# Kernel tuning notes

Measured on AMD Instinct MI355X. Metric: run time of the kernel, lower is better.

The kernel has to match this reference:

```python
import jax, jax.numpy as jnp
import numpy as np

D_MODEL = 1024
NUM_HEADS = 16
DEPTH = D_MODEL // NUM_HEADS  # 64
B, S = 4, 2048
NEG_BIG = -1000000000.0


def setup_inputs() -> dict:
    key = jax.random.key(0)
    ks = jax.random.split(key, 9)
    # Glorot-uniform per-head projection weights, stacked over heads: [H, d_model, depth]
    lim_qkv = np.sqrt(6.0 / (D_MODEL + DEPTH)).astype(np.float32)
    lim_o = np.sqrt(6.0 / (D_MODEL + D_MODEL)).astype(np.float32)
    x = jax.random.normal(ks[0], (B, S, D_MODEL), dtype=jnp.float32)
    attention_mask = jnp.ones((B, S, 1), dtype=jnp.float32)
    Wq = jax.random.uniform(ks[1], (NUM_HEADS, D_MODEL, DEPTH), jnp.float32, -lim_qkv, lim_qkv)
    Wk = jax.random.uniform(ks[2], (NUM_HEADS, D_MODEL, DEPTH), jnp.float32, -lim_qkv, lim_qkv)
    Wv = jax.random.uniform(ks[3], (NUM_HEADS, D_MODEL, DEPTH), jnp.float32, -lim_qkv, lim_qkv)
    bq = jnp.zeros((NUM_HEADS, DEPTH), jnp.float32)
    bk = jnp.zeros((NUM_HEADS, DEPTH), jnp.float32)
    bv = jnp.zeros((NUM_HEADS, DEPTH), jnp.float32)
    Wo = jax.random.uniform(ks[4], (D_MODEL, D_MODEL), jnp.float32, -lim_o, lim_o)
    bo = jnp.zeros((D_MODEL,), jnp.float32)
    return {"x": x, "attention_mask": attention_mask, "Wq": Wq, "bq": bq,
            "Wk": Wk, "bk": bk, "Wv": Wv, "bv": bv, "Wo": Wo, "bo": bo}


def reference(x, attention_mask, Wq, bq, Wk, bk, Wv, bv, Wo, bo):
    # Batched over heads (same math as the per-head Python loop + concat).
    # x: [B,S,D]; Wq/Wk/Wv: [H,D,depth]; bq/bk/bv: [H,depth]
    q = jnp.einsum('bsd,hde->bhse', x, Wq) + bq[None, :, None, :]
    k = jnp.einsum('bsd,hde->bhse', x, Wk) + bk[None, :, None, :]
    v = jnp.einsum('bsd,hde->bhse', x, Wv) + bv[None, :, None, :]
    scale = 1.0 / jnp.sqrt(jnp.asarray(DEPTH, dtype=x.dtype))
    scores = jnp.einsum('bhse,bhte->bhst', q, k) * scale  # [B,H,S,S]
    # original: mask.transpose(-2,-1) -> [B,1,S], broadcast over query rows; add head axis
    mask_t = jnp.swapaxes(attention_mask, -2, -1)[:, None]  # [B,1,1,S]
    scores = scores + (1.0 - mask_t) * NEG_BIG
    probs = jax.nn.softmax(scores, axis=-1)
    z = jnp.einsum('bhst,bhte->bhse', probs, v)  # [B,H,S,depth]
    # concat heads along feature dim (head order matches torch.cat order)
    multi_head = jnp.transpose(z, (0, 2, 1, 3)).reshape(x.shape[0], x.shape[1], NUM_HEADS * DEPTH)
    return multi_head @ Wo + bo
```

## Files before the change

### kernel.cpp

```cpp
#include <hip/hip_runtime.h>

#define NH 16
#define DEP 64
#define DM 1024
#define BB 4
#define SS 2048

typedef __attribute__((ext_vector_type(8))) __bf16 bf16x8;
typedef __attribute__((ext_vector_type(4))) __bf16 bf16x4;
typedef __attribute__((ext_vector_type(2))) __bf16 bf16x2;
typedef __attribute__((ext_vector_type(4))) float f32x4;
typedef __attribute__((ext_vector_type(4))) unsigned u32x4;
typedef __attribute__((ext_vector_type(2))) unsigned u32x2;
typedef unsigned short u16;

#define MFMA_BF16(A, B, C) __builtin_amdgcn_mfma_f32_16x16x32_bf16(A, B, C, 0, 0, 0)

#define SCL 0.18033688011112042f
#define LOG2E 1.4426950408889634f

__device__ __forceinline__ u16 f2bf(float f) {
  unsigned u = __builtin_bit_cast(unsigned, f);
  u += 0x7fffu + ((u >> 16) & 1u);
  return (u16)(u >> 16);
}

__device__ __forceinline__ unsigned pk2(float a, float b) {
  bf16x2 t;
  t[0] = (__bf16)a; t[1] = (__bf16)b;
  return __builtin_bit_cast(unsigned, t);
}

__device__ __forceinline__ void gload_lds16(const u16* g, u16* l) {
  __builtin_amdgcn_global_load_lds((const __attribute__((address_space(1))) void*)g,
                                   (__attribute__((address_space(3))) void*)l, 16, 0, 0);
}

__global__ __launch_bounds__(256) void k_cvt_x(const float* __restrict__ x, u16* __restrict__ xb) {
  int i = (blockIdx.x * 256 + threadIdx.x) * 4;
  float4 v = *(const float4*)(x + i);
  ushort4 o;
  o.x = f2bf(v.x); o.y = f2bf(v.y); o.z = f2bf(v.z); o.w = f2bf(v.w);
  *(ushort4*)(xb + i) = o;
}

__global__ __launch_bounds__(256) void k_pack_qkv(const float* __restrict__ Wq, const float* __restrict__ Wk,
                                                  const float* __restrict__ Wv,
                                                  const float* __restrict__ bq, const float* __restrict__ bk,
                                                  const float* __restrict__ bv,
                                                  u16* __restrict__ wt, float* __restrict__ biasN) {
  __shared__ float lt[64][65];
  int k0 = blockIdx.x * 64;
  int z = blockIdx.y;
  int which = z >> 4, h = z & 15;
  const float* W = which == 0 ? Wq : (which == 1 ? Wk : Wv);
  const float* bsrc = which == 0 ? bq : (which == 1 ? bk : bv);
  const float* src = W + (size_t)h * DM * DEP;
  int t = threadIdx.x;
#pragma unroll
  for (int p = 0; p < 16; ++p) {
    int li = p * 256 + t;
    int r = li >> 6, c = li & 63;
    lt[r][c] = src[(size_t)(k0 + r) * 64 + c];
  }
  __syncthreads();
  int woff = which * DM + h * 64;
#pragma unroll
  for (int p = 0; p < 16; ++p) {
    int li = p * 256 + t;
    int r = li >> 6, c = li & 63;
    wt[(size_t)(woff + r) * DM + k0 + c] = f2bf(lt[c][r]);
  }
  if (blockIdx.x == 0 && t < 64) biasN[woff + t] = bsrc[h * 64 + t];
}

__global__ __launch_bounds__(256) void k_pack_wo(const float* __restrict__ Wo, u16* __restrict__ wot) {
  __shared__ float lt[64][65];
  int k0 = blockIdx.x * 64, n0 = blockIdx.y * 64;
  int t = threadIdx.x;
#pragma unroll
  for (int p = 0; p < 16; ++p) {
    int li = p * 256 + t;
    int r = li >> 6, c = li & 63;
    lt[r][c] = Wo[(size_t)(k0 + r) * DM + n0 + c];
  }
  __syncthreads();
#pragma unroll
  for (int p = 0; p < 16; ++p) {
    int li = p * 256 + t;
    int r = li >> 6, c = li & 63;
    wot[(size_t)(n0 + r) * DM + k0 + c] = f2bf(lt[c][r]);
  }
}

__global__ __launch_bounds__(256) void k_maskbias(const float* __restrict__ mask, float* __restrict__ mb) {
  int i = blockIdx.x * 256 + threadIdx.x;
  mb[i] = (1.0f - mask[i]) * (-1000000000.0f * LOG2E);
}

__global__ __launch_bounds__(256) void k_gemm_qkv(const u16* __restrict__ xb, const u16* __restrict__ wt,
                                                  const float* __restrict__ biasN,
                                                  u16* __restrict__ qb, u16* __restrict__ kb,
                                                  u16* __restrict__ vtb) {
  __shared__ u16 lA[2][128 * 32];
  __shared__ u16 lB[2][128 * 32];
  const int tid = threadIdx.x;
  const int lane = tid & 63, w = tid >> 6;
  const int m0 = blockIdx.x * 128, n0 = blockIdx.y * 128;
  const int wm = (w >> 1) * 64, wn = (w & 1) * 64;
  const int fr = lane & 15, fg = lane >> 4;
  const int bidx = tid * 16;
  const int row0 = bidx >> 6, c0 = (bidx & 63) >> 1;
  f32x4 acc[4][4] = {};
  auto stage = [&](int k0, int buf) {
    gload_lds16(xb + (size_t)(m0 + row0) * DM + k0 + c0, &lA[buf][w * 512]);
    gload_lds16(xb + (size_t)(m0 + row0 + 64) * DM + k0 + c0, &lA[buf][2048 + w * 512]);
    gload_lds16(wt + (size_t)(n0 + row0) * DM + k0 + c0, &lB[buf][w * 512]);
    gload_lds16(wt + (size_t)(n0 + row0 + 64) * DM + k0 + c0, &lB[buf][2048 + w * 512]);
  };
  stage(0, 0);
  __syncthreads();
  for (int k0 = 0; k0 < DM; k0 += 32) {
    const int cur = (k0 >> 5) & 1;
    if (k0 + 32 < DM) stage(k0 + 32, cur ^ 1);
    bf16x8 af[4], bfr[4];
#pragma unroll
    for (int i = 0; i < 4; ++i) {
      af[i] = *(const bf16x8*)&lA[cur][(wm + i * 16 + fr) * 32 + fg * 8];
      bfr[i] = *(const bf16x8*)&lB[cur][(wn + i * 16 + fr) * 32 + fg * 8];
    }
#pragma unroll
    for (int i = 0; i < 4; ++i)
#pragma unroll
      for (int j = 0; j < 4; ++j)
        acc[i][j] = MFMA_BF16(af[i], bfr[j], acc[i][j]);
    __syncthreads();
  }
#pragma unroll
  for (int i = 0; i < 4; ++i)
#pragma unroll
    for (int j = 0; j < 4; ++j) {
      int n = n0 + wn + j * 16 + fr;
      float bn = biasN[n];
      int which = n >> 10, rem = n & 1023, h = rem >> 6, d = rem & 63;
#pragma unroll
      for (int r = 0; r < 4; ++r) {
        int m = m0 + wm + i * 16 + fg * 4 + r;
        int b = m >> 11, s = m & 2047;
        float val = acc[i][j][r] + bn;
        if (which == 0)      qb[(((size_t)(b * NH + h) * SS + s) << 6) + d] = f2bf(val * SCL);
        else if (which == 1) kb[(((size_t)(b * NH + h) * SS + s) << 6) + d] = f2bf(val);
        else                 vtb[(((size_t)(b * NH + h) * 64 + d) << 11) + s] = f2bf(val);
      }
    }
}

__global__ __launch_bounds__(256, 2) void k_attn(const u16* __restrict__ qb, const u16* __restrict__ kb,
                                                 const u16* __restrict__ vtb, const float* __restrict__ mbias,
                                                 u16* __restrict__ zb) {
  __shared__ u16 sK[2][64 * 64];
  __shared__ u16 sV[2][64 * 64];
  const int bid = blockIdx.x;
  const int sw = (bid & 7) * 64 + (bid >> 3);
  const int bh = sw >> 3;
  const int qx = sw & 7;
  const int b = bh >> 4, h = bh & 15;
  const int tid = threadIdx.x, lane = tid & 63, w = tid >> 6;
  const int q0 = qx * 256 + w * 64;
  const u16* Q  = qb  + (size_t)bh * SS * 64;
  const u16* K  = kb  + (size_t)bh * SS * 64;
  const u16* VT = vtb + (size_t)bh * 64 * SS;
  const float* mbb = mbias + b * SS;
  const int fr = lane & 15, fg = lane >> 4;
  const int fr7 = fr & 7;
  const int rsub = lane >> 3;
  const int cg = (lane & 7) ^ rsub;
  const int kc0 = (fg ^ fr7) * 16;
  const int kc1 = ((4 + fg) ^ fr7) * 16;
  const int fg1 = fg >> 1, fgb = (fg & 1) * 8;
  const int cX0 = (((fg1)     ^ fr7)) * 16 + fgb;
  const int cX1 = (((2 + (fg1 ^ 1)) ^ fr7)) * 16 + fgb;
  const int cY0 = (((4 + fg1) ^ fr7)) * 16 + fgb;
  const int cY1 = (((6 + (fg1 ^ 1)) ^ fr7)) * 16 + fgb;
  bf16x8 qlo[4], qhi[4];
#pragma unroll
  for (int qf = 0; qf < 4; ++qf) {
    qlo[qf] = *(const bf16x8*)&Q[(q0 + 16 * qf + fr) * 64 + fg * 8];
    qhi[qf] = *(const bf16x8*)&Q[(q0 + 16 * qf + fr) * 64 + 32 + fg * 8];
  }
  float lrun[4] = {0.f, 0.f, 0.f, 0.f};
  f32x4 o[4][4] = {};

#pragma unroll
  for (int j = 0; j < 2; ++j) {
    int i = w * 2 + j;
    gload_lds16(K + (size_t)(8 * i + rsub) * 64 + cg * 8, &sK[0][i * 512]);
    gload_lds16(VT + (size_t)(8 * i + rsub) * SS + cg * 8, &sV[0][i * 512]);
  }
  __syncthreads();

  for (int t = 0; t < 32; ++t) {
    const int cur = t & 1;
    if (t < 31) {
      const int kvn = (t + 1) * 64;
#pragma unroll
      for (int j = 0; j < 2; ++j) {
        int i = w * 2 + j;
        gload_lds16(K + (size_t)(kvn + 8 * i + rsub) * 64 + cg * 8, &sK[cur ^ 1][i * 512]);
        gload_lds16(VT + (size_t)(8 * i + rsub) * SS + kvn + cg * 8, &sV[cur ^ 1][i * 512]);
      }
    }
    const int kv = t * 64;
    const char* Kb = (const char*)&sK[cur][0];
    const char* Vb = (const char*)&sV[cur][0];
    bf16x8 klo[4], khi[4];
#pragma unroll
    for (int kt = 0; kt < 4; ++kt) {
      klo[kt] = *(const bf16x8*)(Kb + (kt * 16 + fr) * 128 + kc0);
      khi[kt] = *(const bf16x8*)(Kb + (kt * 16 + fr) * 128 + kc1);
    }
    u32x2 vx0[4], vx1[4], vy0[4], vy1[4];
#pragma unroll
    for (int dc = 0; dc < 4; ++dc) {
      const char* rb = Vb + (dc * 16 + fr) * 128;
      vx0[dc] = *(const u32x2*)(rb + cX0);
      vx1[dc] = *(const u32x2*)(rb + cX1);
      vy0[dc] = *(const u32x2*)(rb + cY0);
      vy1[dc] = *(const u32x2*)(rb + cY1);
    }
#pragma unroll
    for (int qf = 0; qf < 4; ++qf) {
      f32x4 sc[4];
      __builtin_amdgcn_s_setprio(1);
#pragma unroll
      for (int kt = 0; kt < 4; ++kt) {
        f32x4 mb4 = *(const f32x4*)(mbb + kv + kt * 16 + fg * 4);
        sc[kt] = MFMA_BF16(khi[kt], qhi[qf], MFMA_BF16(klo[kt], qlo[qf], mb4));
      }
      __builtin_amdgcn_s_setprio(0);
      float e00 = __builtin_amdgcn_exp2f(sc[0][0]), e01 = __builtin_amdgcn_exp2f(sc[0][1]);
      float e02 = __builtin_amdgcn_exp2f(sc[0][2]), e03 = __builtin_amdgcn_exp2f(sc[0][3]);
      float e10 = __builtin_amdgcn_exp2f(sc[1][0]), e11 = __builtin_amdgcn_exp2f(sc[1][1]);
      float e12 = __builtin_amdgcn_exp2f(sc[1][2]), e13 = __builtin_amdgcn_exp2f(sc[1][3]);
      float e20 = __builtin_amdgcn_exp2f(sc[2][0]), e21 = __builtin_amdgcn_exp2f(sc[2][1]);
      float e22 = __builtin_amdgcn_exp2f(sc[2][2]), e23 = __builtin_amdgcn_exp2f(sc[2][3]);
      float e30 = __builtin_amdgcn_exp2f(sc[3][0]), e31 = __builtin_amdgcn_exp2f(sc[3][1]);
      float e32 = __builtin_amdgcn_exp2f(sc[3][2]), e33 = __builtin_amdgcn_exp2f(sc[3][3]);
      lrun[qf] += ((e00 + e01) + (e02 + e03)) + ((e10 + e11) + (e12 + e13))
                + ((e20 + e21) + (e22 + e23)) + ((e30 + e31) + (e32 + e33));
      unsigned w00 = pk2(e00, e01), w01 = pk2(e02, e03);
      unsigned w10 = pk2(e10, e11), w11 = pk2(e12, e13);
      unsigned w20 = pk2(e20, e21), w21 = pk2(e22, e23);
      unsigned w30 = pk2(e30, e31), w31 = pk2(e32, e33);
      unsigned x2 = (unsigned)__shfl_xor((int)w10, 32);
      unsigned x3 = (unsigned)__shfl_xor((int)w11, 32);
      unsigned y2 = (unsigned)__shfl_xor((int)w30, 32);
      unsigned y3 = (unsigned)__shfl_xor((int)w31, 32);
      u32x4 ux = {w00, w01, x2, x3};
      u32x4 uy = {w20, w21, y2, y3};
      bf16x8 paX = __builtin_bit_cast(bf16x8, ux);
      bf16x8 paY = __builtin_bit_cast(bf16x8, uy);
      __builtin_amdgcn_s_setprio(1);
#pragma unroll
      for (int dc = 0; dc < 4; ++dc) {
        u32x4 vxw = {vx0[dc][0], vx0[dc][1], vx1[dc][0], vx1[dc][1]};
        u32x4 vyw = {vy0[dc][0], vy0[dc][1], vy1[dc][0], vy1[dc][1]};
        bf16x8 vX = __builtin_bit_cast(bf16x8, vxw);
        bf16x8 vY = __builtin_bit_cast(bf16x8, vyw);
        o[qf][dc] = MFMA_BF16(paX, vX, o[qf][dc]);
        o[qf][dc] = MFMA_BF16(paY, vY, o[qf][dc]);
      }
      __builtin_amdgcn_s_setprio(0);
    }
    __syncthreads();
  }
#pragma unroll
  for (int qf = 0; qf < 4; ++qf) {
    float l = lrun[qf];
    l += __shfl_xor(l, 16);
    l += __shfl_xor(l, 32);
#pragma unroll
    for (int r = 0; r < 4; ++r) {
      float linv = 1.0f / __shfl(l, 4 * fg + r);
      int s = q0 + 16 * qf + 4 * fg + r;
#pragma unroll
      for (int dc = 0; dc < 4; ++dc)
        zb[(size_t)(b * SS + s) * DM + h * 64 + dc * 16 + fr] = f2bf(o[qf][dc][r] * linv);
    }
  }
}

__global__ __launch_bounds__(256) void k_gemm_out(const u16* __restrict__ zb, const u16* __restrict__ wot,
                                                  const float* __restrict__ bo, float* __restrict__ out) {
  __shared__ u16 lA[2][128 * 32];
  __shared__ u16 lB[2][128 * 32];
  const int tid = threadIdx.x;
  const int lane = tid & 63, w = tid >> 6;
  const int m0 = blockIdx.x * 128, n0 = blockIdx.y * 128;
  const int wm = (w >> 1) * 64, wn = (w & 1) * 64;
  const int fr = lane & 15, fg = lane >> 4;
  const int bidx = tid * 16;
  const int row0 = bidx >> 6, c0 = (bidx & 63) >> 1;
  f32x4 acc[4][4] = {};
  auto stage = [&](int k0, int buf) {
    gload_lds16(zb + (size_t)(m0 + row0) * DM + k0 + c0, &lA[buf][w * 512]);
    gload_lds16(zb + (size_t)(m0 + row0 + 64) * DM + k0 + c0, &lA[buf][2048 + w * 512]);
    gload_lds16(wot + (size_t)(n0 + row0) * DM + k0 + c0, &lB[buf][w * 512]);
    gload_lds16(wot + (size_t)(n0 + row0 + 64) * DM + k0 + c0, &lB[buf][2048 + w * 512]);
  };
  stage(0, 0);
  __syncthreads();
  for (int k0 = 0; k0 < DM; k0 += 32) {
    const int cur = (k0 >> 5) & 1;
    if (k0 + 32 < DM) stage(k0 + 32, cur ^ 1);
    bf16x8 af[4], bfr[4];
#pragma unroll
    for (int i = 0; i < 4; ++i) {
      af[i] = *(const bf16x8*)&lA[cur][(wm + i * 16 + fr) * 32 + fg * 8];
      bfr[i] = *(const bf16x8*)&lB[cur][(wn + i * 16 + fr) * 32 + fg * 8];
    }
#pragma unroll
    for (int i = 0; i < 4; ++i)
#pragma unroll
      for (int j = 0; j < 4; ++j)
        acc[i][j] = MFMA_BF16(af[i], bfr[j], acc[i][j]);
    __syncthreads();
  }
#pragma unroll
  for (int i = 0; i < 4; ++i)
#pragma unroll
    for (int j = 0; j < 4; ++j) {
      int n = n0 + wn + j * 16 + fr;
      float bn = bo[n];
#pragma unroll
      for (int r = 0; r < 4; ++r) {
        int m = m0 + wm + i * 16 + fg * 4 + r;
        out[(size_t)m * DM + n] = acc[i][j][r] + bn;
      }
    }
}

extern "C" void kernel_launch(void* const* d_in, const int* in_sizes, int n_in,
                              void* d_out, int out_size, void* d_ws, size_t ws_size,
                              hipStream_t stream) {
  const float* x    = (const float*)d_in[0];
  const float* mask = (const float*)d_in[1];
  const float* Wq   = (const float*)d_in[2];
  const float* bq   = (const float*)d_in[3];
  const float* Wk   = (const float*)d_in[4];
  const float* bk   = (const float*)d_in[5];
  const float* Wv   = (const float*)d_in[6];
  const float* bv   = (const float*)d_in[7];
  const float* Wo   = (const float*)d_in[8];
  const float* bo   = (const float*)d_in[9];
  char* ws = (char*)d_ws;
  u16*   xb    = (u16*)(ws + 0);
  u16*   zb    = xb;
  u16*   wt    = (u16*)(ws + 16777216);
  u16*   wot   = (u16*)(ws + 23068672);
  float* biasN = (float*)(ws + 25165824);
  float* mb    = (float*)(ws + 25178112);
  u16*   qb    = (u16*)(ws + 25210880);
  u16*   kb    = (u16*)(ws + 41988096);
  u16*   vtb   = (u16*)(ws + 58765312);
  float* out   = (float*)d_out;

  k_cvt_x<<<dim3(8192), dim3(256), 0, stream>>>(x, xb);
  k_pack_qkv<<<dim3(16, 48), dim3(256), 0, stream>>>(Wq, Wk, Wv, bq, bk, bv, wt, biasN);
  k_pack_wo<<<dim3(16, 16), dim3(256), 0, stream>>>(Wo, wot);
  k_maskbias<<<dim3(32), dim3(256), 0, stream>>>(mask, mb);
  k_gemm_qkv<<<dim3(64, 24), dim3(256), 0, stream>>>(xb, wt, biasN, qb, kb, vtb);
  k_attn<<<dim3(512), dim3(256), 0, stream>>>(qb, kb, vtb, mb, zb);
  k_gemm_out<<<dim3(64, 8), dim3(256), 0, stream>>>(zb, wot, bo, out);
}
```

Measured before the change: 213.4 us.

## Merge prep kernels into one launch and software-pipeline QK/softmax-PV in attention

Four small preprocessing kernels (x conversion, QKV weight pack, Wo pack, mask bias) are merged into a single launch that dispatches on block index, removing three kernel launches and their gaps. In the attention loop, the mask-bias loads are hoisted out of the per-query-fragment loop and the V fragments are pre-assembled once per tile. The QK MFMAs for the next query fragment are interleaved with the exp/PV work of the current one to overlap matrix and vector work. This adds register pressure from a second score buffer, which could hurt occupancy.

```diff
diff --git a/kernel.cpp b/kernel.cpp
--- a/kernel.cpp
+++ b/kernel.cpp
@@ -36,66 +36,66 @@
                                    (__attribute__((address_space(3))) void*)l, 16, 0, 0);
 }
 
-__global__ __launch_bounds__(256) void k_cvt_x(const float* __restrict__ x, u16* __restrict__ xb) {
-  int i = (blockIdx.x * 256 + threadIdx.x) * 4;
-  float4 v = *(const float4*)(x + i);
-  ushort4 o;
-  o.x = f2bf(v.x); o.y = f2bf(v.y); o.z = f2bf(v.z); o.w = f2bf(v.w);
-  *(ushort4*)(xb + i) = o;
-}
-
-__global__ __launch_bounds__(256) void k_pack_qkv(const float* __restrict__ Wq, const float* __restrict__ Wk,
-                                                  const float* __restrict__ Wv,
-                                                  const float* __restrict__ bq, const float* __restrict__ bk,
-                                                  const float* __restrict__ bv,
-                                                  u16* __restrict__ wt, float* __restrict__ biasN) {
+__global__ __launch_bounds__(256) void k_prep(const float* __restrict__ x, const float* __restrict__ mask,
+                                              const float* __restrict__ Wq, const float* __restrict__ Wk,
+                                              const float* __restrict__ Wv,
+                                              const float* __restrict__ bq, const float* __restrict__ bk,
+                                              const float* __restrict__ bv, const float* __restrict__ Wo,
+                                              u16* __restrict__ xb, u16* __restrict__ wt,
+                                              u16* __restrict__ wot, float* __restrict__ biasN,
+                                              float* __restrict__ mb) {
   __shared__ float lt[64][65];
-  int k0 = blockIdx.x * 64;
-  int z = blockIdx.y;
-  int which = z >> 4, h = z & 15;
-  const float* W = which == 0 ? Wq : (which == 1 ? Wk : Wv);
-  const float* bsrc = which == 0 ? bq : (which == 1 ? bk : bv);
-  const float* src = W + (size_t)h * DM * DEP;
-  int t = threadIdx.x;
-#pragma unroll
-  for (int p = 0; p < 16; ++p) {
-    int li = p * 256 + t;
-    int r = li >> 6, c = li & 63;
-    lt[r][c] = src[(size_t)(k0 + r) * 64 + c];
-  }
-  __syncthreads();
-  int woff = which * DM + h * 64;
-#pragma unroll
-  for (int p = 0; p < 16; ++p) {
-    int li = p * 256 + t;
-    int r = li >> 6, c = li & 63;
-    wt[(size_t)(woff + r) * DM + k0 + c] = f2bf(lt[c][r]);
-  }
-  if (blockIdx.x == 0 && t < 64) biasN[woff + t] = bsrc[h * 64 + t];
-}
-
-__global__ __launch_bounds__(256) void k_pack_wo(const float* __restrict__ Wo, u16* __restrict__ wot) {
-  __shared__ float lt[64][65];
-  int k0 = blockIdx.x * 64, n0 = blockIdx.y * 64;
-  int t = threadIdx.x;
-#pragma unroll
-  for (int p = 0; p < 16; ++p) {
-    int li = p * 256 + t;
-    int r = li >> 6, c = li & 63;
-    lt[r][c] = Wo[(size_t)(k0 + r) * DM + n0 + c];
-  }
-  __syncthreads();
-#pragma unroll
-  for (int p = 0; p < 16; ++p) {
-    int li = p * 256 + t;
-    int r = li >> 6, c = li & 63;
-    wot[(size_t)(n0 + r) * DM + k0 + c] = f2bf(lt[c][r]);
-  }
-}
-
-__global__ __launch_bounds__(256) void k_maskbias(const float* __restrict__ mask, float* __restrict__ mb) {
-  int i = blockIdx.x * 256 + threadIdx.x;
-  mb[i] = (1.0f - mask[i]) * (-1000000000.0f * LOG2E);
+  const int bidg = blockIdx.x;
+  const int t = threadIdx.x;
+  if (bidg < 8192) {
+    int i = (bidg * 256 + t) * 4;
+    float4 v = *(const float4*)(x + i);
+    ushort4 o;
+    o.x = f2bf(v.x); o.y = f2bf(v.y); o.z = f2bf(v.z); o.w = f2bf(v.w);
+    *(ushort4*)(xb + i) = o;
+  } else if (bidg < 8960) {
+    int z = bidg - 8192;
+    int kx = z & 15, zy = z >> 4;
+    int which = zy >> 4, h = zy & 15;
+    int k0 = kx * 64;
+    const float* W = which == 0 ? Wq : (which == 1 ? Wk : Wv);
+    const float* bsrc = which == 0 ? bq : (which == 1 ? bk : bv);
+    const float* src = W + (size_t)h * DM * DEP;
+#pragma unroll
+    for (int p = 0; p < 16; ++p) {
+      int li = p * 256 + t;
+      int r = li >> 6, c = li & 63;
+      lt[r][c] = src[(size_t)(k0 + r) * 64 + c];
+    }
+    __syncthreads();
+    int woff = which * DM + h * 64;
+#pragma unroll
+    for (int p = 0; p < 16; ++p) {
+      int li = p * 256 + t;
+      int r = li >> 6, c = li & 63;
+      wt[(size_t)(woff + r) * DM + k0 + c] = f2bf(lt[c][r]);
+    }
+    if (kx == 0 && t < 64) biasN[woff + t] = bsrc[h * 64 + t];
+  } else if (bidg < 9216) {
+    int z = bidg - 8960;
+    int k0 = (z & 15) * 64, n0 = (z >> 4) * 64;
+#pragma unroll
+    for (int p = 0; p < 16; ++p) {
+      int li = p * 256 + t;
+      int r = li >> 6, c = li & 63;
+      lt[r][c] = Wo[(size_t)(k0 + r) * DM + n0 + c];
+    }
+    __syncthreads();
+#pragma unroll
+    for (int p = 0; p < 16; ++p) {
+      int li = p * 256 + t;
+      int r = li >> 6, c = li & 63;
+      wot[(size_t)(n0 + r) * DM + k0 + c] = f2bf(lt[c][r]);
+    }
+  } else {
+    int i = (bidg - 9216) * 256 + t;
+    mb[i] = (1.0f - mask[i]) * (-1000000000.0f * LOG2E);
+  }
 }
 
 __global__ __launch_bounds__(256) void k_gemm_qkv(const u16* __restrict__ xb, const u16* __restrict__ wt,
@@ -213,31 +213,37 @@
     const int kv = t * 64;
     const char* Kb = (const char*)&sK[cur][0];
     const char* Vb = (const char*)&sV[cur][0];
+    f32x4 mbv[4];
+#pragma unroll
+    for (int kt = 0; kt < 4; ++kt) mbv[kt] = *(const f32x4*)(mbb + kv + kt * 16 + fg * 4);
     bf16x8 klo[4], khi[4];
 #pragma unroll
     for (int kt = 0; kt < 4; ++kt) {
       klo[kt] = *(const bf16x8*)(Kb + (kt * 16 + fr) * 128 + kc0);
       khi[kt] = *(const bf16x8*)(Kb + (kt * 16 + fr) * 128 + kc1);
     }
-    u32x2 vx0[4], vx1[4], vy0[4], vy1[4];
+    bf16x8 vX[4], vY[4];
 #pragma unroll
     for (int dc = 0; dc < 4; ++dc) {
       const char* rb = Vb + (dc * 16 + fr) * 128;
-      vx0[dc] = *(const u32x2*)(rb + cX0);
-      vx1[dc] = *(const u32x2*)(rb + cX1);
-      vy0[dc] = *(const u32x2*)(rb + cY0);
-      vy1[dc] = *(const u32x2*)(rb + cY1);
-    }
-#pragma unroll
-    for (int qf = 0; qf < 4; ++qf) {
-      f32x4 sc[4];
+      u32x2 a0 = *(const u32x2*)(rb + cX0);
+      u32x2 a1 = *(const u32x2*)(rb + cX1);
+      u32x2 b0 = *(const u32x2*)(rb + cY0);
+      u32x2 b1 = *(const u32x2*)(rb + cY1);
+      u32x4 ua = {a0[0], a0[1], a1[0], a1[1]};
+      u32x4 ub = {b0[0], b0[1], b1[0], b1[1]};
+      vX[dc] = __builtin_bit_cast(bf16x8, ua);
+      vY[dc] = __builtin_bit_cast(bf16x8, ub);
+    }
+
+    auto QKf = [&](int qf, f32x4 (&sc)[4]) {
       __builtin_amdgcn_s_setprio(1);
 #pragma unroll
-      for (int kt = 0; kt < 4; ++kt) {
-        f32x4 mb4 = *(const f32x4*)(mbb + kv + kt * 16 + fg * 4);
-        sc[kt] = MFMA_BF16(khi[kt], qhi[qf], MFMA_BF16(klo[kt], qlo[qf], mb4));
-      }
+      for (int kt = 0; kt < 4; ++kt)
+        sc[kt] = MFMA_BF16(khi[kt], qhi[qf], MFMA_BF16(klo[kt], qlo[qf], mbv[kt]));
       __builtin_amdgcn_s_setprio(0);
+    };
+    auto SMPV = [&](int qf, f32x4 (&sc)[4]) {
       float e00 = __builtin_amdgcn_exp2f(sc[0][0]), e01 = __builtin_amdgcn_exp2f(sc[0][1]);
       float e02 = __builtin_amdgcn_exp2f(sc[0][2]), e03 = __builtin_amdgcn_exp2f(sc[0][3]);
       float e10 = __builtin_amdgcn_exp2f(sc[1][0]), e11 = __builtin_amdgcn_exp2f(sc[1][1]);
@@ -263,15 +269,19 @@
       __builtin_amdgcn_s_setprio(1);
 #pragma unroll
       for (int dc = 0; dc < 4; ++dc) {
-        u32x4 vxw = {vx0[dc][0], vx0[dc][1], vx1[dc][0], vx1[dc][1]};
-        u32x4 vyw = {vy0[dc][0], vy0[dc][1], vy1[dc][0], vy1[dc][1]};
-        bf16x8 vX = __builtin_bit_cast(bf16x8, vxw);
-        bf16x8 vY = __builtin_bit_cast(bf16x8, vyw);
-        o[qf][dc] = MFMA_BF16(paX, vX, o[qf][dc]);
-        o[qf][dc] = MFMA_BF16(paY, vY, o[qf][dc]);
+        o[qf][dc] = MFMA_BF16(paX, vX[dc], o[qf][dc]);
+        o[qf][dc] = MFMA_BF16(paY, vY[dc], o[qf][dc]);
       }
       __builtin_amdgcn_s_setprio(0);
-    }
+    };
+
+    f32x4 scA[4], scB[4];
+    QKf(0, scA);
+    QKf(1, scB); SMPV(0, scA);
+    QKf(2, scA); SMPV(1, scB);
+    QKf(3, scB); SMPV(2, scA);
+    SMPV(3, scB);
+
     __syncthreads();
   }
 #pragma unroll
@@ -365,10 +375,8 @@
   u16*   vtb   = (u16*)(ws + 58765312);
   float* out   = (float*)d_out;
 
-  k_cvt_x<<<dim3(8192), dim3(256), 0, stream>>>(x, xb);
-  k_pack_qkv<<<dim3(16, 48), dim3(256), 0, stream>>>(Wq, Wk, Wv, bq, bk, bv, wt, biasN);
-  k_pack_wo<<<dim3(16, 16), dim3(256), 0, stream>>>(Wo, wot);
-  k_maskbias<<<dim3(32), dim3(256), 0, stream>>>(mask, mb);
+  k_prep<<<dim3(9248), dim3(256), 0, stream>>>(x, mask, Wq, Wk, Wv, bq, bk, bv, Wo,
+                                               xb, wt, wot, biasN, mb);
   k_gemm_qkv<<<dim3(64, 24), dim3(256), 0, stream>>>(xb, wt, biasN, qb, kb, vtb);
   k_attn<<<dim3(512), dim3(256), 0, stream>>>(qb, kb, vtb, mb, zb);
   k_gemm_out<<<dim3(64, 8), dim3(256), 0, stream>>>(zb, wot, bo, out);
```

New measurement: 216.8 us. Within noise of the previous version (+1.6%).
